# Kernel tuning notes

Hardware: AMD Instinct MI355X
Metric: run time of the kernel (lower is better)

The kernel has to match this reference:

```python
import jax, jax.numpy as jnp
import numpy as np

PH = PW = 16  # patch size


def setup_inputs() -> dict:
    key = jax.random.key(0)
    k1, k2, k3, k4, k5 = jax.random.split(key, 5)
    B, N, D, V = 8, 4096, 768, 10240
    x = jax.random.uniform(k1, (B, N, D), dtype=jnp.float32)          # (B, N, ph*pw*C) in [0,1)
    patch_coord = jax.random.randint(k2, (B, N, 2), 0, 64).astype(jnp.int64)  # (y, x) grid coords
    patch_valid = jax.random.randint(k3, (B, N), 0, 2).astype(bool)
    proj_w = jax.random.normal(k4, (D, D), dtype=jnp.float32) * 0.02  # Linear weight (out, in), no bias
    pos_table = jax.random.normal(k5, (2, V, D), dtype=jnp.float32) * 0.02
    return {"x": x, "patch_coord": patch_coord, "patch_valid": patch_valid,
            "proj_w": proj_w, "pos_table": pos_table}


def reference(x, patch_coord, patch_valid, proj_w, pos_table):
    B, N, PPC = x.shape
    C = PPC // (PH * PW)
    # Reorder patch pixels from (ph, pw, C) flat order to (C, ph, pw) flat order.
    x = x.reshape(B, N, PH, PW, C).transpose(0, 1, 4, 2, 3).reshape(B, N, PPC)
    x = 2.0 * (x - 0.5)
    x = jnp.einsum('bnk,dk->bnd', x, proj_w)  # Linear, bias=False
    # External (y, x) -> internal (x, y)
    position_ids = patch_coord[..., ::-1]
    clamped = jnp.maximum(position_ids, 0)
    # Equivalent to one_hot(clamped) @ table summed over the 2 coord axes.
    pos = pos_table[0][clamped[..., 0]] + pos_table[1][clamped[..., 1]]  # (B, N, D)
    padding_positions = ~patch_valid
    pos = jnp.where(padding_positions[..., None], 0.0, pos)
    return x + pos, position_ids, padding_positions
```

## Files before the change

### kernel.cpp

```cpp
#include <hip/hip_runtime.h>
#include <hip/hip_bf16.h>
#include <cstddef>

#define D_DIM 768
#define V_DIM 10240
#define ROWS 32768
#define BM 128
#define BN 128
#define BK 32

using bf16x8 = __attribute__((ext_vector_type(8))) __bf16;
using f32x4  = __attribute__((ext_vector_type(4))) float;

__global__ void prep_w(const float* __restrict__ W, __bf16* __restrict__ Wp,
                       float* __restrict__ bias) {
    int d = blockIdx.x;
    int t = threadIdx.x;
    float s = 0.f;
    for (int j = t; j < D_DIM; j += 256) {
        int c  = j % 3;
        int pw = (j / 3) & 15;
        int ph = j / 48;
        int k  = c * 256 + ph * 16 + pw;
        float w = W[d * D_DIM + k];
        Wp[d * D_DIM + j] = (__bf16)(2.0f * w);
        s += w;
    }
    __shared__ float red[256];
    red[t] = s;
    __syncthreads();
    for (int off = 128; off > 0; off >>= 1) {
        if (t < off) red[t] += red[t + off];
        __syncthreads();
    }
    if (t == 0) bias[d] = -red[0];
}

__global__ void conv_aux(const float* __restrict__ X, __bf16* __restrict__ Xb,
                         const int* __restrict__ coord, const int* __restrict__ valid,
                         float* __restrict__ out1, float* __restrict__ out2) {
    int i = blockIdx.x * blockDim.x + threadIdx.x;
    size_t base = (size_t)i * 8;
    const float4* src = (const float4*)(X + base);
    float4 f0 = src[0];
    float4 f1 = src[1];
    bf16x8 v;
    v[0] = (__bf16)f0.x; v[1] = (__bf16)f0.y; v[2] = (__bf16)f0.z; v[3] = (__bf16)f0.w;
    v[4] = (__bf16)f1.x; v[5] = (__bf16)f1.y; v[6] = (__bf16)f1.z; v[7] = (__bf16)f1.w;
    *(bf16x8*)(Xb + base) = v;

    if (i < ROWS) {
        int c0 = coord[2 * i];
        int c1 = coord[2 * i + 1];
        out1[2 * i]     = (float)c1;
        out1[2 * i + 1] = (float)c0;
        out2[i] = valid[i] ? 0.0f : 1.0f;
    }
}

__global__ void aux_out(const int* __restrict__ coord, const int* __restrict__ valid,
                        float* __restrict__ out1, float* __restrict__ out2) {
    int i = blockIdx.x * blockDim.x + threadIdx.x;
    if (i < ROWS) {
        int c0 = coord[2 * i];
        int c1 = coord[2 * i + 1];
        out1[2 * i]     = (float)c1;
        out1[2 * i + 1] = (float)c0;
        out2[i] = valid[i] ? 0.0f : 1.0f;
    }
}

__launch_bounds__(256)
__global__ void gemm_fast(const __bf16* __restrict__ Xb, const __bf16* __restrict__ Wp,
                          const float* __restrict__ bias, const float* __restrict__ ptab,
                          const int* __restrict__ coord, const int* __restrict__ valid,
                          float* __restrict__ out) {
    __shared__ __align__(16) __bf16 la[BM * BK];
    __shared__ __align__(16) __bf16 lb[BN * BK];

    const int n0 = blockIdx.x * BN;
    const int m0 = blockIdx.y * BM;

    const int tid  = threadIdx.x;
    const int lane = tid & 63;
    const int wave = tid >> 6;
    const int wr   = (wave >> 1) * 64;
    const int wc   = (wave & 1) * 64;
    const int lr   = lane & 15;
    const int kq   = (lane >> 4) * 8;

    f32x4 acc[4][4] = {};

    for (int kt = 0; kt < D_DIM / BK; ++kt) {
        const int k0 = kt * BK;

        #pragma unroll
        for (int i = 0; i < 2; ++i) {
            int idx = i * 2048 + tid * 8;
            int row = idx >> 5;
            int col = idx & 31;
            const __bf16* srcA = Xb + (size_t)(m0 + row) * D_DIM + k0 + col;
            __builtin_amdgcn_global_load_lds(
                (const __attribute__((address_space(1))) void*)srcA,
                (__attribute__((address_space(3))) void*)&la[idx], 16, 0, 0);
            const __bf16* srcB = Wp + (size_t)(n0 + row) * D_DIM + k0 + col;
            __builtin_amdgcn_global_load_lds(
                (const __attribute__((address_space(1))) void*)srcB,
                (__attribute__((address_space(3))) void*)&lb[idx], 16, 0, 0);
        }

        __syncthreads();

        bf16x8 af[4], bfr[4];
        #pragma unroll
        for (int i = 0; i < 4; ++i)
            af[i] = *(const bf16x8*)&la[(wr + i * 16 + lr) * BK + kq];
        #pragma unroll
        for (int j = 0; j < 4; ++j)
            bfr[j] = *(const bf16x8*)&lb[(wc + j * 16 + lr) * BK + kq];

        #pragma unroll
        for (int i = 0; i < 4; ++i)
            #pragma unroll
            for (int j = 0; j < 4; ++j)
                acc[i][j] = __builtin_amdgcn_mfma_f32_16x16x32_bf16(af[i], bfr[j], acc[i][j], 0, 0, 0);

        __syncthreads();
    }

    const float* pt0 = ptab;
    const float* pt1 = ptab + (size_t)V_DIM * D_DIM;
    const int rq = (lane >> 4) * 4;

    float bvals[4];
    #pragma unroll
    for (int j = 0; j < 4; ++j)
        bvals[j] = bias[n0 + wc + j * 16 + lr];

    #pragma unroll
    for (int i = 0; i < 4; ++i) {
        #pragma unroll
        for (int r = 0; r < 4; ++r) {
            int m = m0 + wr + i * 16 + rq + r;
            int c0 = coord[2 * m];
            int c1 = coord[2 * m + 1];
            if (c0 < 0) c0 = 0;
            if (c1 < 0) c1 = 0;
            int vld = valid[m];
            #pragma unroll
            for (int j = 0; j < 4; ++j) {
                int d = n0 + wc + j * 16 + lr;
                float v = acc[i][j][r] + bvals[j];
                if (vld)
                    v += pt0[(size_t)c1 * D_DIM + d] + pt1[(size_t)c0 * D_DIM + d];
                out[(size_t)m * D_DIM + d] = v;
            }
        }
    }
}

__launch_bounds__(256)
__global__ void gemm_slow(const float* __restrict__ X, const __bf16* __restrict__ Wp,
                          const float* __restrict__ bias, const float* __restrict__ ptab,
                          const int* __restrict__ coord, const int* __restrict__ valid,
                          float* __restrict__ out) {
    __shared__ __align__(16) __bf16 la[BM * BK];
    __shared__ __align__(16) __bf16 lb[BN * BK];

    const int n0 = blockIdx.x * BN;
    const int m0 = blockIdx.y * BM;

    const int tid  = threadIdx.x;
    const int lane = tid & 63;
    const int wave = tid >> 6;
    const int wr   = (wave >> 1) * 64;
    const int wc   = (wave & 1) * 64;
    const int lr   = lane & 15;
    const int kq   = (lane >> 4) * 8;

    f32x4 acc[4][4] = {};

    for (int kt = 0; kt < D_DIM / BK; ++kt) {
        const int k0 = kt * BK;

        #pragma unroll
        for (int i = 0; i < 2; ++i) {
            int idx = i * 2048 + tid * 8;
            int row = idx >> 5;
            int col = idx & 31;
            const __bf16* src = Wp + (size_t)(n0 + row) * D_DIM + k0 + col;
            __builtin_amdgcn_global_load_lds(
                (const __attribute__((address_space(1))) void*)src,
                (__attribute__((address_space(3))) void*)&lb[idx], 16, 0, 0);
        }

        #pragma unroll
        for (int i = 0; i < 2; ++i) {
            int idx = i * 2048 + tid * 8;
            int row = idx >> 5;
            int col = idx & 31;
            const float4* src = (const float4*)(X + (size_t)(m0 + row) * D_DIM + k0 + col);
            float4 f0 = src[0];
            float4 f1 = src[1];
            bf16x8 v;
            v[0] = (__bf16)f0.x; v[1] = (__bf16)f0.y; v[2] = (__bf16)f0.z; v[3] = (__bf16)f0.w;
            v[4] = (__bf16)f1.x; v[5] = (__bf16)f1.y; v[6] = (__bf16)f1.z; v[7] = (__bf16)f1.w;
            *(bf16x8*)&la[idx] = v;
        }

        __syncthreads();

        bf16x8 af[4], bfr[4];
        #pragma unroll
        for (int i = 0; i < 4; ++i)
            af[i] = *(const bf16x8*)&la[(wr + i * 16 + lr) * BK + kq];
        #pragma unroll
        for (int j = 0; j < 4; ++j)
            bfr[j] = *(const bf16x8*)&lb[(wc + j * 16 + lr) * BK + kq];

        #pragma unroll
        for (int i = 0; i < 4; ++i)
            #pragma unroll
            for (int j = 0; j < 4; ++j)
                acc[i][j] = __builtin_amdgcn_mfma_f32_16x16x32_bf16(af[i], bfr[j], acc[i][j], 0, 0, 0);

        __syncthreads();
    }

    const float* pt0 = ptab;
    const float* pt1 = ptab + (size_t)V_DIM * D_DIM;
    const int rq = (lane >> 4) * 4;

    float bvals[4];
    #pragma unroll
    for (int j = 0; j < 4; ++j)
        bvals[j] = bias[n0 + wc + j * 16 + lr];

    #pragma unroll
    for (int i = 0; i < 4; ++i) {
        #pragma unroll
        for (int r = 0; r < 4; ++r) {
            int m = m0 + wr + i * 16 + rq + r;
            int c0 = coord[2 * m];
            int c1 = coord[2 * m + 1];
            if (c0 < 0) c0 = 0;
            if (c1 < 0) c1 = 0;
            int vld = valid[m];
            #pragma unroll
            for (int j = 0; j < 4; ++j) {
                int d = n0 + wc + j * 16 + lr;
                float v = acc[i][j][r] + bvals[j];
                if (vld)
                    v += pt0[(size_t)c1 * D_DIM + d] + pt1[(size_t)c0 * D_DIM + d];
                out[(size_t)m * D_DIM + d] = v;
            }
        }
    }
}

extern "C" void kernel_launch(void* const* d_in, const int* in_sizes, int n_in,
                              void* d_out, int out_size, void* d_ws, size_t ws_size,
                              hipStream_t stream) {
    const float* x     = (const float*)d_in[0];
    const int*   coord = (const int*)d_in[1];
    const int*   valid = (const int*)d_in[2];
    const float* W     = (const float*)d_in[3];
    const float* ptab  = (const float*)d_in[4];

    float* out0 = (float*)d_out;
    float* out1 = out0 + (size_t)ROWS * D_DIM;
    float* out2 = out1 + (size_t)ROWS * 2;

    const size_t xb_bytes = (size_t)ROWS * D_DIM * sizeof(__bf16);
    const size_t wp_bytes = (size_t)D_DIM * D_DIM * sizeof(__bf16);
    const size_t need = xb_bytes + wp_bytes + D_DIM * sizeof(float);

    if (ws_size >= need) {
        __bf16* Xb  = (__bf16*)d_ws;
        __bf16* Wp  = (__bf16*)((char*)d_ws + xb_bytes);
        float* bias = (float*)((char*)d_ws + xb_bytes + wp_bytes);

        hipLaunchKernelGGL(prep_w, dim3(D_DIM), dim3(256), 0, stream, W, Wp, bias);
        hipLaunchKernelGGL(conv_aux, dim3((ROWS * D_DIM / 8) / 256), dim3(256), 0, stream,
                           x, Xb, coord, valid, out1, out2);
        hipLaunchKernelGGL(gemm_fast, dim3(D_DIM / BN, ROWS / BM), dim3(256), 0, stream,
                           Xb, Wp, bias, ptab, coord, valid, out0);
    } else {
        __bf16* Wp  = (__bf16*)d_ws;
        float* bias = (float*)((char*)d_ws + wp_bytes);

        hipLaunchKernelGGL(prep_w, dim3(D_DIM), dim3(256), 0, stream, W, Wp, bias);
        hipLaunchKernelGGL(aux_out, dim3(ROWS / 256), dim3(256), 0, stream, coord, valid, out1, out2);
        hipLaunchKernelGGL(gemm_slow, dim3(D_DIM / BN, ROWS / BM), dim3(256), 0, stream,
                           x, Wp, bias, ptab, coord, valid, out0);
    }
}
```

Baseline: 285.6 us.

## Fuse fp32 conversion into a full-width double-buffered GEMM with swizzled LDS

Result: slower. 293.7 us (+2.8%).

```diff
diff --git a/kernel.cpp b/kernel.cpp
--- a/kernel.cpp
+++ b/kernel.cpp
@@ -4,29 +4,27 @@
 
 #define D_DIM 768
 #define V_DIM 10240
-#define ROWS 32768
-#define BM 128
-#define BN 128
-#define BK 32
+#define ROWS  32768
+#define BM    64
+#define BK    32
+#define KTILES (D_DIM / BK)
 
 using bf16x8 = __attribute__((ext_vector_type(8))) __bf16;
+using bf16x4 = __attribute__((ext_vector_type(4))) __bf16;
 using f32x4  = __attribute__((ext_vector_type(4))) float;
 
 __global__ void prep_w(const float* __restrict__ W, __bf16* __restrict__ Wp,
                        float* __restrict__ bias) {
-    int d = blockIdx.x;
-    int t = threadIdx.x;
+    __shared__ float row[D_DIM];
+    __shared__ float red[256];
+    const int d = blockIdx.x;
+    const int t = threadIdx.x;
     float s = 0.f;
-    for (int j = t; j < D_DIM; j += 256) {
-        int c  = j % 3;
-        int pw = (j / 3) & 15;
-        int ph = j / 48;
-        int k  = c * 256 + ph * 16 + pw;
-        float w = W[d * D_DIM + k];
-        Wp[d * D_DIM + j] = (__bf16)(2.0f * w);
+    for (int k = t; k < D_DIM; k += 256) {
+        float w = W[(size_t)d * D_DIM + k];
+        row[k] = w;
         s += w;
     }
-    __shared__ float red[256];
     red[t] = s;
     __syncthreads();
     for (int off = 128; off > 0; off >>= 1) {
@@ -34,225 +32,147 @@
         __syncthreads();
     }
     if (t == 0) bias[d] = -red[0];
+    for (int j = t; j < D_DIM; j += 256) {
+        int c  = j % 3;
+        int pw = (j / 3) & 15;
+        int ph = j / 48;
+        Wp[(size_t)d * D_DIM + j] = (__bf16)(2.0f * row[c * 256 + ph * 16 + pw]);
+    }
 }
 
-__global__ void conv_aux(const float* __restrict__ X, __bf16* __restrict__ Xb,
-                         const int* __restrict__ coord, const int* __restrict__ valid,
-                         float* __restrict__ out1, float* __restrict__ out2) {
-    int i = blockIdx.x * blockDim.x + threadIdx.x;
-    size_t base = (size_t)i * 8;
-    const float4* src = (const float4*)(X + base);
-    float4 f0 = src[0];
-    float4 f1 = src[1];
-    bf16x8 v;
-    v[0] = (__bf16)f0.x; v[1] = (__bf16)f0.y; v[2] = (__bf16)f0.z; v[3] = (__bf16)f0.w;
-    v[4] = (__bf16)f1.x; v[5] = (__bf16)f1.y; v[6] = (__bf16)f1.z; v[7] = (__bf16)f1.w;
-    *(bf16x8*)(Xb + base) = v;
-
-    if (i < ROWS) {
-        int c0 = coord[2 * i];
-        int c1 = coord[2 * i + 1];
-        out1[2 * i]     = (float)c1;
-        out1[2 * i + 1] = (float)c0;
-        out2[i] = valid[i] ? 0.0f : 1.0f;
-    }
-}
-
-__global__ void aux_out(const int* __restrict__ coord, const int* __restrict__ valid,
-                        float* __restrict__ out1, float* __restrict__ out2) {
-    int i = blockIdx.x * blockDim.x + threadIdx.x;
-    if (i < ROWS) {
-        int c0 = coord[2 * i];
-        int c1 = coord[2 * i + 1];
-        out1[2 * i]     = (float)c1;
-        out1[2 * i + 1] = (float)c0;
-        out2[i] = valid[i] ? 0.0f : 1.0f;
-    }
-}
-
-__launch_bounds__(256)
-__global__ void gemm_fast(const __bf16* __restrict__ Xb, const __bf16* __restrict__ Wp,
-                          const float* __restrict__ bias, const float* __restrict__ ptab,
-                          const int* __restrict__ coord, const int* __restrict__ valid,
-                          float* __restrict__ out) {
-    __shared__ __align__(16) __bf16 la[BM * BK];
-    __shared__ __align__(16) __bf16 lb[BN * BK];
-
-    const int n0 = blockIdx.x * BN;
-    const int m0 = blockIdx.y * BM;
+__launch_bounds__(512, 2)
+__global__ void gemm_fused(const float* __restrict__ X, const __bf16* __restrict__ Wp,
+                           const float* __restrict__ bias, const float* __restrict__ ptab,
+                           const int* __restrict__ coord, const int* __restrict__ valid,
+                           float* __restrict__ out0, float* __restrict__ out1,
+                           float* __restrict__ out2) {
+    __shared__ __align__(16) __bf16 la[2][BM * BK];
+    __shared__ __align__(16) __bf16 lb[2][D_DIM * BK];
 
     const int tid  = threadIdx.x;
     const int lane = tid & 63;
     const int wave = tid >> 6;
-    const int wr   = (wave >> 1) * 64;
-    const int wc   = (wave & 1) * 64;
+    const int wr   = (wave >> 2) * 32;
+    const int wc   = (wave & 3) * 192;
     const int lr   = lane & 15;
-    const int kq   = (lane >> 4) * 8;
-
-    f32x4 acc[4][4] = {};
-
-    for (int kt = 0; kt < D_DIM / BK; ++kt) {
-        const int k0 = kt * BK;
+    const int qh   = lane >> 4;
+
+    const int m0 = blockIdx.x * BM;
+
+    if (tid < BM) {
+        int m  = m0 + tid;
+        int c0 = coord[2 * m];
+        int c1 = coord[2 * m + 1];
+        out1[2 * m]     = (float)c1;
+        out1[2 * m + 1] = (float)c0;
+        out2[m] = valid[m] ? 0.0f : 1.0f;
+    }
+
+    const __bf16* bsrc[6];
+    int bdst[6];
+    #pragma unroll
+    for (int i = 0; i < 6; ++i) {
+        int q   = i * 512 + tid;
+        int row = q >> 2;
+        int su  = (q & 3) ^ ((row >> 1) & 3);
+        bsrc[i] = Wp + (size_t)row * D_DIM + su * 8;
+        bdst[i] = q * 8;
+    }
+
+    const int a_row = tid >> 3;
+    const int a_u   = (tid & 7) >> 1;
+    const int a_h   = tid & 1;
+    const int a_off = a_row * BK + (a_u ^ ((a_row >> 1) & 3)) * 8 + a_h * 4;
+    const float* aptr = X + (size_t)(m0 + a_row) * D_DIM + ((tid & 7) << 2);
+
+    int aoff[2], boff[12];
+    #pragma unroll
+    for (int i = 0; i < 2; ++i) {
+        int row = wr + i * 16 + lr;
+        aoff[i] = row * BK + (qh ^ ((row >> 1) & 3)) * 8;
+    }
+    #pragma unroll
+    for (int j = 0; j < 12; ++j) {
+        int row = wc + j * 16 + lr;
+        boff[j] = row * BK + (qh ^ ((row >> 1) & 3)) * 8;
+    }
+
+    f32x4 acc[2][12] = {};
+
+    #pragma unroll
+    for (int i = 0; i < 6; ++i)
+        __builtin_amdgcn_global_load_lds(
+            (const __attribute__((address_space(1))) void*)bsrc[i],
+            (__attribute__((address_space(3))) void*)&lb[0][bdst[i]], 16, 0, 0);
+    {
+        float4 f = *(const float4*)aptr;
+        bf16x4 v;
+        v[0] = (__bf16)f.x; v[1] = (__bf16)f.y; v[2] = (__bf16)f.z; v[3] = (__bf16)f.w;
+        *(bf16x4*)&la[0][a_off] = v;
+    }
+    __syncthreads();
+
+    for (int kt = 0; kt < KTILES; ++kt) {
+        const int cur = kt & 1;
+        const int nxt = cur ^ 1;
+        const int k1  = (kt + 1) * BK;
+
+        float4 fA;
+        if (kt + 1 < KTILES) {
+            #pragma unroll
+            for (int i = 0; i < 6; ++i)
+                __builtin_amdgcn_global_load_lds(
+                    (const __attribute__((address_space(1))) void*)(bsrc[i] + k1),
+                    (__attribute__((address_space(3))) void*)&lb[nxt][bdst[i]], 16, 0, 0);
+            fA = *(const float4*)(aptr + k1);
+        }
+
+        bf16x8 af0 = *(const bf16x8*)&la[cur][aoff[0]];
+        bf16x8 af1 = *(const bf16x8*)&la[cur][aoff[1]];
 
         #pragma unroll
-        for (int i = 0; i < 2; ++i) {
-            int idx = i * 2048 + tid * 8;
-            int row = idx >> 5;
-            int col = idx & 31;
-            const __bf16* srcA = Xb + (size_t)(m0 + row) * D_DIM + k0 + col;
-            __builtin_amdgcn_global_load_lds(
-                (const __attribute__((address_space(1))) void*)srcA,
-                (__attribute__((address_space(3))) void*)&la[idx], 16, 0, 0);
-            const __bf16* srcB = Wp + (size_t)(n0 + row) * D_DIM + k0 + col;
-            __builtin_amdgcn_global_load_lds(
-                (const __attribute__((address_space(1))) void*)srcB,
-                (__attribute__((address_space(3))) void*)&lb[idx], 16, 0, 0);
-        }
-
-        __syncthreads();
-
-        bf16x8 af[4], bfr[4];
-        #pragma unroll
-        for (int i = 0; i < 4; ++i)
-            af[i] = *(const bf16x8*)&la[(wr + i * 16 + lr) * BK + kq];
-        #pragma unroll
-        for (int j = 0; j < 4; ++j)
-            bfr[j] = *(const bf16x8*)&lb[(wc + j * 16 + lr) * BK + kq];
-
-        #pragma unroll
-        for (int i = 0; i < 4; ++i)
-            #pragma unroll
-            for (int j = 0; j < 4; ++j)
-                acc[i][j] = __builtin_amdgcn_mfma_f32_16x16x32_bf16(af[i], bfr[j], acc[i][j], 0, 0, 0);
-
+        for (int j = 0; j < 12; ++j) {
+            bf16x8 bfv = *(const bf16x8*)&lb[cur][boff[j]];
+            acc[0][j] = __builtin_amdgcn_mfma_f32_16x16x32_bf16(af0, bfv, acc[0][j], 0, 0, 0);
+            acc[1][j] = __builtin_amdgcn_mfma_f32_16x16x32_bf16(af1, bfv, acc[1][j], 0, 0, 0);
+        }
+
+        if (kt + 1 < KTILES) {
+            bf16x4 v;
+            v[0] = (__bf16)fA.x; v[1] = (__bf16)fA.y; v[2] = (__bf16)fA.z; v[3] = (__bf16)fA.w;
+            *(bf16x4*)&la[nxt][a_off] = v;
+        }
         __syncthreads();
     }
 
     const float* pt0 = ptab;
     const float* pt1 = ptab + (size_t)V_DIM * D_DIM;
-    const int rq = (lane >> 4) * 4;
-
-    float bvals[4];
-    #pragma unroll
-    for (int j = 0; j < 4; ++j)
-        bvals[j] = bias[n0 + wc + j * 16 + lr];
-
-    #pragma unroll
-    for (int i = 0; i < 4; ++i) {
+
+    float bv[12];
+    #pragma unroll
+    for (int j = 0; j < 12; ++j)
+        bv[j] = bias[wc + j * 16 + lr];
+
+    #pragma unroll
+    for (int i = 0; i < 2; ++i) {
         #pragma unroll
         for (int r = 0; r < 4; ++r) {
-            int m = m0 + wr + i * 16 + rq + r;
+            const int m = m0 + wr + i * 16 + qh * 4 + r;
             int c0 = coord[2 * m];
             int c1 = coord[2 * m + 1];
             if (c0 < 0) c0 = 0;
             if (c1 < 0) c1 = 0;
-            int vld = valid[m];
+            const int vld = valid[m];
+            const float* p0 = pt0 + (size_t)c1 * D_DIM;
+            const float* p1 = pt1 + (size_t)c0 * D_DIM;
+            float* orow = out0 + (size_t)m * D_DIM;
             #pragma unroll
-            for (int j = 0; j < 4; ++j) {
-                int d = n0 + wc + j * 16 + lr;
-                float v = acc[i][j][r] + bvals[j];
+            for (int j = 0; j < 12; ++j) {
+                const int d = wc + j * 16 + lr;
+                float v = acc[i][j][r] + bv[j];
                 if (vld)
-                    v += pt0[(size_t)c1 * D_DIM + d] + pt1[(size_t)c0 * D_DIM + d];
-                out[(size_t)m * D_DIM + d] = v;
-            }
-        }
-    }
-}
-
-__launch_bounds__(256)
-__global__ void gemm_slow(const float* __restrict__ X, const __bf16* __restrict__ Wp,
-                          const float* __restrict__ bias, const float* __restrict__ ptab,
-                          const int* __restrict__ coord, const int* __restrict__ valid,
-                          float* __restrict__ out) {
-    __shared__ __align__(16) __bf16 la[BM * BK];
-    __shared__ __align__(16) __bf16 lb[BN * BK];
-
-    const int n0 = blockIdx.x * BN;
-    const int m0 = blockIdx.y * BM;
-
-    const int tid  = threadIdx.x;
-    const int lane = tid & 63;
-    const int wave = tid >> 6;
-    const int wr   = (wave >> 1) * 64;
-    const int wc   = (wave & 1) * 64;
-    const int lr   = lane & 15;
-    const int kq   = (lane >> 4) * 8;
-
-    f32x4 acc[4][4] = {};
-
-    for (int kt = 0; kt < D_DIM / BK; ++kt) {
-        const int k0 = kt * BK;
-
-        #pragma unroll
-        for (int i = 0; i < 2; ++i) {
-            int idx = i * 2048 + tid * 8;
-            int row = idx >> 5;
-            int col = idx & 31;
-            const __bf16* src = Wp + (size_t)(n0 + row) * D_DIM + k0 + col;
-            __builtin_amdgcn_global_load_lds(
-                (const __attribute__((address_space(1))) void*)src,
-                (__attribute__((address_space(3))) void*)&lb[idx], 16, 0, 0);
-        }
-
-        #pragma unroll
-        for (int i = 0; i < 2; ++i) {
-            int idx = i * 2048 + tid * 8;
-            int row = idx >> 5;
-            int col = idx & 31;
-            const float4* src = (const float4*)(X + (size_t)(m0 + row) * D_DIM + k0 + col);
-            float4 f0 = src[0];
-            float4 f1 = src[1];
-            bf16x8 v;
-            v[0] = (__bf16)f0.x; v[1] = (__bf16)f0.y; v[2] = (__bf16)f0.z; v[3] = (__bf16)f0.w;
-            v[4] = (__bf16)f1.x; v[5] = (__bf16)f1.y; v[6] = (__bf16)f1.z; v[7] = (__bf16)f1.w;
-            *(bf16x8*)&la[idx] = v;
-        }
-
-        __syncthreads();
-
-        bf16x8 af[4], bfr[4];
-        #pragma unroll
-        for (int i = 0; i < 4; ++i)
-            af[i] = *(const bf16x8*)&la[(wr + i * 16 + lr) * BK + kq];
-        #pragma unroll
-        for (int j = 0; j < 4; ++j)
-            bfr[j] = *(const bf16x8*)&lb[(wc + j * 16 + lr) * BK + kq];
-
-        #pragma unroll
-        for (int i = 0; i < 4; ++i)
-            #pragma unroll
-            for (int j = 0; j < 4; ++j)
-                acc[i][j] = __builtin_amdgcn_mfma_f32_16x16x32_bf16(af[i], bfr[j], acc[i][j], 0, 0, 0);
-
-        __syncthreads();
-    }
-
-    const float* pt0 = ptab;
-    const float* pt1 = ptab + (size_t)V_DIM * D_DIM;
-    const int rq = (lane >> 4) * 4;
-
-    float bvals[4];
-    #pragma unroll
-    for (int j = 0; j < 4; ++j)
-        bvals[j] = bias[n0 + wc + j * 16 + lr];
-
-    #pragma unroll
-    for (int i = 0; i < 4; ++i) {
-        #pragma unroll
-        for (int r = 0; r < 4; ++r) {
-            int m = m0 + wr + i * 16 + rq + r;
-            int c0 = coord[2 * m];
-            int c1 = coord[2 * m + 1];
-            if (c0 < 0) c0 = 0;
-            if (c1 < 0) c1 = 0;
-            int vld = valid[m];
-            #pragma unroll
-            for (int j = 0; j < 4; ++j) {
-                int d = n0 + wc + j * 16 + lr;
-                float v = acc[i][j][r] + bvals[j];
-                if (vld)
-                    v += pt0[(size_t)c1 * D_DIM + d] + pt1[(size_t)c0 * D_DIM + d];
-                out[(size_t)m * D_DIM + d] = v;
+                    v += p0[d] + p1[d];
+                orow[d] = v;
             }
         }
     }
@@ -271,27 +191,10 @@
     float* out1 = out0 + (size_t)ROWS * D_DIM;
     float* out2 = out1 + (size_t)ROWS * 2;
 
-    const size_t xb_bytes = (size_t)ROWS * D_DIM * sizeof(__bf16);
-    const size_t wp_bytes = (size_t)D_DIM * D_DIM * sizeof(__bf16);
-    const size_t need = xb_bytes + wp_bytes + D_DIM * sizeof(float);
-
-    if (ws_size >= need) {
-        __bf16* Xb  = (__bf16*)d_ws;
-        __bf16* Wp  = (__bf16*)((char*)d_ws + xb_bytes);
-        float* bias = (float*)((char*)d_ws + xb_bytes + wp_bytes);
-
-        hipLaunchKernelGGL(prep_w, dim3(D_DIM), dim3(256), 0, stream, W, Wp, bias);
-        hipLaunchKernelGGL(conv_aux, dim3((ROWS * D_DIM / 8) / 256), dim3(256), 0, stream,
-                           x, Xb, coord, valid, out1, out2);
-        hipLaunchKernelGGL(gemm_fast, dim3(D_DIM / BN, ROWS / BM), dim3(256), 0, stream,
-                           Xb, Wp, bias, ptab, coord, valid, out0);
-    } else {
-        __bf16* Wp  = (__bf16*)d_ws;
-        float* bias = (float*)((char*)d_ws + wp_bytes);
-
-        hipLaunchKernelGGL(prep_w, dim3(D_DIM), dim3(256), 0, stream, W, Wp, bias);
-        hipLaunchKernelGGL(aux_out, dim3(ROWS / 256), dim3(256), 0, stream, coord, valid, out1, out2);
-        hipLaunchKernelGGL(gemm_slow, dim3(D_DIM / BN, ROWS / BM), dim3(256), 0, stream,
-                           x, Wp, bias, ptab, coord, valid, out0);
-    }
+    __bf16* Wp   = (__bf16*)d_ws;
+    float*  bias = (float*)((char*)d_ws + (size_t)D_DIM * D_DIM * sizeof(__bf16));
+
+    hipLaunchKernelGGL(prep_w, dim3(D_DIM), dim3(256), 0, stream, W, Wp, bias);
+    hipLaunchKernelGGL(gemm_fused, dim3(ROWS / BM), dim3(512), 0, stream,
+                       x, Wp, bias, ptab, coord, valid, out0, out1, out2);
 }
```

## Swizzle LDS tiles, remap GEMM blocks per XCD, coalesce weight prep reads

Applied to the files above, without the earlier changes.

New measurement: 274.3 us. -4.0%, faster.

```diff
diff --git a/kernel.cpp b/kernel.cpp
--- a/kernel.cpp
+++ b/kernel.cpp
@@ -14,26 +14,29 @@
 
 __global__ void prep_w(const float* __restrict__ W, __bf16* __restrict__ Wp,
                        float* __restrict__ bias) {
-    int d = blockIdx.x;
-    int t = threadIdx.x;
+    __shared__ float row[D_DIM];
+    __shared__ float red[256];
+    const int d = blockIdx.x;
+    const int t = threadIdx.x;
     float s = 0.f;
+    for (int k = t; k < D_DIM; k += 256) {
+        float w = W[(size_t)d * D_DIM + k];
+        row[k] = w;
+        s += w;
+    }
+    red[t] = s;
+    __syncthreads();
+    for (int off = 128; off > 0; off >>= 1) {
+        if (t < off) red[t] += red[t + off];
+        __syncthreads();
+    }
+    if (t == 0) bias[d] = -red[0];
     for (int j = t; j < D_DIM; j += 256) {
         int c  = j % 3;
         int pw = (j / 3) & 15;
         int ph = j / 48;
-        int k  = c * 256 + ph * 16 + pw;
-        float w = W[d * D_DIM + k];
-        Wp[d * D_DIM + j] = (__bf16)(2.0f * w);
-        s += w;
-    }
-    __shared__ float red[256];
-    red[t] = s;
-    __syncthreads();
-    for (int off = 128; off > 0; off >>= 1) {
-        if (t < off) red[t] += red[t + off];
-        __syncthreads();
-    }
-    if (t == 0) bias[d] = -red[0];
+        Wp[(size_t)d * D_DIM + j] = (__bf16)(2.0f * row[c * 256 + ph * 16 + pw]);
+    }
 }
 
 __global__ void conv_aux(const float* __restrict__ X, __bf16* __restrict__ Xb,
@@ -78,8 +81,13 @@
     __shared__ __align__(16) __bf16 la[BM * BK];
     __shared__ __align__(16) __bf16 lb[BN * BK];
 
-    const int n0 = blockIdx.x * BN;
-    const int m0 = blockIdx.y * BM;
+    const int id  = blockIdx.x;
+    const int xcd = id & 7;
+    const int j6  = id >> 3;
+    const int p   = xcd * 32 + j6 / 6;
+    const int c   = j6 % 6;
+    const int m0  = p * BM;
+    const int n0  = c * BN;
 
     const int tid  = threadIdx.x;
     const int lane = tid & 63;
@@ -87,7 +95,29 @@
     const int wr   = (wave >> 1) * 64;
     const int wc   = (wave & 1) * 64;
     const int lr   = lane & 15;
-    const int kq   = (lane >> 4) * 8;
+    const int qh   = lane >> 4;
+
+    const __bf16* srcA[2];
+    const __bf16* srcB[2];
+    int dst[2];
+    #pragma unroll
+    for (int i = 0; i < 2; ++i) {
+        int q   = i * 256 + tid;
+        int row = q >> 2;
+        int un  = (q & 3) ^ ((row >> 1) & 3);
+        srcA[i] = Xb + (size_t)(m0 + row) * D_DIM + un * 8;
+        srcB[i] = Wp + (size_t)(n0 + row) * D_DIM + un * 8;
+        dst[i]  = q * 8;
+    }
+
+    int aoff[4], boff[4];
+    #pragma unroll
+    for (int i = 0; i < 4; ++i) {
+        int rowa = wr + i * 16 + lr;
+        aoff[i] = rowa * BK + ((qh ^ ((rowa >> 1) & 3)) * 8);
+        int rowb = wc + i * 16 + lr;
+        boff[i] = rowb * BK + ((qh ^ ((rowb >> 1) & 3)) * 8);
+    }
 
     f32x4 acc[4][4] = {};
 
@@ -96,17 +126,12 @@
 
         #pragma unroll
         for (int i = 0; i < 2; ++i) {
-            int idx = i * 2048 + tid * 8;
-            int row = idx >> 5;
-            int col = idx & 31;
-            const __bf16* srcA = Xb + (size_t)(m0 + row) * D_DIM + k0 + col;
             __builtin_amdgcn_global_load_lds(
-                (const __attribute__((address_space(1))) void*)srcA,
-                (__attribute__((address_space(3))) void*)&la[idx], 16, 0, 0);
-            const __bf16* srcB = Wp + (size_t)(n0 + row) * D_DIM + k0 + col;
+                (const __attribute__((address_space(1))) void*)(srcA[i] + k0),
+                (__attribute__((address_space(3))) void*)&la[dst[i]], 16, 0, 0);
             __builtin_amdgcn_global_load_lds(
-                (const __attribute__((address_space(1))) void*)srcB,
-                (__attribute__((address_space(3))) void*)&lb[idx], 16, 0, 0);
+                (const __attribute__((address_space(1))) void*)(srcB[i] + k0),
+                (__attribute__((address_space(3))) void*)&lb[dst[i]], 16, 0, 0);
         }
 
         __syncthreads();
@@ -114,10 +139,10 @@
         bf16x8 af[4], bfr[4];
         #pragma unroll
         for (int i = 0; i < 4; ++i)
-            af[i] = *(const bf16x8*)&la[(wr + i * 16 + lr) * BK + kq];
+            af[i] = *(const bf16x8*)&la[aoff[i]];
         #pragma unroll
         for (int j = 0; j < 4; ++j)
-            bfr[j] = *(const bf16x8*)&lb[(wc + j * 16 + lr) * BK + kq];
+            bfr[j] = *(const bf16x8*)&lb[boff[j]];
 
         #pragma unroll
         for (int i = 0; i < 4; ++i)
@@ -283,7 +308,7 @@
         hipLaunchKernelGGL(prep_w, dim3(D_DIM), dim3(256), 0, stream, W, Wp, bias);
         hipLaunchKernelGGL(conv_aux, dim3((ROWS * D_DIM / 8) / 256), dim3(256), 0, stream,
                            x, Xb, coord, valid, out1, out2);
-        hipLaunchKernelGGL(gemm_fast, dim3(D_DIM / BN, ROWS / BM), dim3(256), 0, stream,
+        hipLaunchKernelGGL(gemm_fast, dim3((ROWS / BM) * (D_DIM / BN)), dim3(256), 0, stream,
                            Xb, Wp, bias, ptab, coord, valid, out0);
     } else {
         __bf16* Wp  = (__bf16*)d_ws;
```
